# Kernel optimization log

Measured on AMD Instinct MI355X. Metric: run time of the kernel, lower is better.

## Reference

```python
import jax, jax.numpy as jnp
import numpy as np

D_MODEL = 1024
NUM_HEADS = 16
D_HEAD = D_MODEL // NUM_HEADS
BATCH = 4
SEQ = 2048
NEG_INF = -1e30


def setup_inputs() -> dict:
    key = jax.random.key(0)
    k_x, k_q, k_k, k_v, k_o = jax.random.split(key, 5)
    scale = 1.0 / np.sqrt(D_MODEL)
    x = jax.random.normal(k_x, (BATCH, SEQ, D_MODEL), dtype=jnp.float32)
    Qw = jax.random.normal(k_q, (D_MODEL, D_MODEL), dtype=jnp.float32) * scale
    Kw = jax.random.normal(k_k, (D_MODEL, D_MODEL), dtype=jnp.float32) * scale
    Vw = jax.random.normal(k_v, (D_MODEL, D_MODEL), dtype=jnp.float32) * scale
    Ow = jax.random.normal(k_o, (D_MODEL, D_MODEL), dtype=jnp.float32) * scale
    padding_mask = jnp.zeros((BATCH, SEQ), dtype=bool)  # True = masked position
    return {"x": x, "Qw": Qw, "Kw": Kw, "Vw": Vw, "Ow": Ow, "padding_mask": padding_mask}


def reference(x, Qw, Kw, Vw, Ow, padding_mask):
    B, S, D = x.shape
    H, dh = NUM_HEADS, D_HEAD
    # torch Linear (no bias): y = x @ W.T
    q = jnp.einsum("bsd,ed->bse", x, Qw).reshape(B, S, H, dh)
    k = jnp.einsum("bsd,ed->bse", x, Kw).reshape(B, S, H, dh)
    v = jnp.einsum("bsd,ed->bse", x, Vw).reshape(B, S, H, dh)
    # scores: [B, H, Sq, Sk]
    score = jnp.einsum("bqhd,bkhd->bhqk", q, k) / jnp.sqrt(jnp.float32(dh))
    # causal mask (masked=True)
    causal = jnp.tril(jnp.ones((S, S), dtype=bool))  # True = keep
    score = jnp.where(causal[None, None, :, :], score, NEG_INF)
    # padding mask: True = masked key position
    score = jnp.where(padding_mask[:, None, None, :], NEG_INF, score)
    attn = jax.nn.softmax(score, axis=-1)  # dropout=0.0 (eval mode)
    ctx = jnp.einsum("bhqk,bkhd->bqhd", attn, v).reshape(B, S, D)
    out = jnp.einsum("bsd,ed->bse", ctx, Ow)
    return out
```

## Files before the change

kernel.cpp:

```cpp
#include <hip/hip_runtime.h>
#include <hip/hip_bf16.h>

typedef __attribute__((ext_vector_type(8))) short short8;
typedef __attribute__((ext_vector_type(4))) float f32x4;

#define MFMA_BF16_16x16x32(a,b,c) __builtin_amdgcn_mfma_f32_16x16x32_bf16((a),(b),(c),0,0,0)

constexpr int B_  = 4;
constexpr int S_  = 2048;
constexpr int H_  = 16;
constexpr int DH_ = 64;
constexpr int D_  = 1024;
constexpr int M_  = B_ * S_;

__device__ __forceinline__ unsigned short f2bf(float f) {
  union { float f; unsigned u; } v; v.f = f;
  unsigned u = v.u;
  u += 0x7fffu + ((u >> 16) & 1u);
  return (unsigned short)(u >> 16);
}

__device__ __forceinline__ short8 cvt8(f32x4 a, f32x4 b) {
  union { __hip_bfloat162 h[4]; short8 s; } u;
  u.h[0] = __float22bfloat162_rn(make_float2(a[0], a[1]));
  u.h[1] = __float22bfloat162_rn(make_float2(a[2], a[3]));
  u.h[2] = __float22bfloat162_rn(make_float2(b[0], b[1]));
  u.h[3] = __float22bfloat162_rn(make_float2(b[2], b[3]));
  return u.s;
}

__global__ __launch_bounds__(256)
void gemm_qkv(const float* __restrict__ x,
              const float* __restrict__ Qw, const float* __restrict__ Kw,
              const float* __restrict__ Vw,
              unsigned short* __restrict__ Qo, unsigned short* __restrict__ Ko,
              unsigned short* __restrict__ VTo) {
  constexpr int BM = 128, BK = 32, LDK = 40;
  __shared__ __align__(16) short As[BM * LDK];
  __shared__ __align__(16) short Bs[BM * LDK];

  const int nb = blockIdx.x;
  const float* W;
  unsigned short* out;
  float scale = 1.0f;
  int epi;
  if (nb < 8)       { W = Qw; out = Qo;  scale = 0.125f; epi = 1; }
  else if (nb < 16) { W = Kw; out = Ko;  epi = 1; }
  else              { W = Vw; out = VTo; epi = 2; }

  const int tid  = threadIdx.x;
  const int lane = tid & 63;
  const int w    = tid >> 6;
  const int quad = lane >> 4;
  const int l16  = lane & 15;
  const int wm   = (w >> 1) * 64;
  const int wn   = (w & 1) * 64;

  const int m0 = blockIdx.y * BM;
  const int n0 = (nb & 7) * 128;

  f32x4 acc[4][4];
  #pragma unroll
  for (int i = 0; i < 4; ++i)
    #pragma unroll
    for (int j = 0; j < 4; ++j)
      acc[i][j] = (f32x4){0.f, 0.f, 0.f, 0.f};

  for (int k0 = 0; k0 < D_; k0 += BK) {
    __syncthreads();
    #pragma unroll
    for (int i = 0; i < 2; ++i) {
      int flat = i * 256 + tid;
      int row  = flat >> 2;
      int col  = (flat & 3) * 8;
      const float* Ap = x + (size_t)(m0 + row) * D_ + k0 + col;
      *(short8*)(&As[row * LDK + col]) = cvt8(*(const f32x4*)Ap, *(const f32x4*)(Ap + 4));
      const float* Wp = W + (size_t)(n0 + row) * D_ + k0 + col;
      *(short8*)(&Bs[row * LDK + col]) = cvt8(*(const f32x4*)Wp, *(const f32x4*)(Wp + 4));
    }
    __syncthreads();

    short8 af[4], bf[4];
    #pragma unroll
    for (int i = 0; i < 4; ++i)
      af[i] = *(const short8*)(&As[(wm + i * 16 + l16) * LDK + quad * 8]);
    #pragma unroll
    for (int j = 0; j < 4; ++j)
      bf[j] = *(const short8*)(&Bs[(wn + j * 16 + l16) * LDK + quad * 8]);
    #pragma unroll
    for (int i = 0; i < 4; ++i)
      #pragma unroll
      for (int j = 0; j < 4; ++j)
        acc[i][j] = MFMA_BF16_16x16x32(af[i], bf[j], acc[i][j]);
  }

  #pragma unroll
  for (int i = 0; i < 4; ++i)
    #pragma unroll
    for (int j = 0; j < 4; ++j)
      #pragma unroll
      for (int r = 0; r < 4; ++r) {
        int m = m0 + wm + i * 16 + quad * 4 + r;
        int n = n0 + wn + j * 16 + l16;
        unsigned short bv = f2bf(acc[i][j][r] * scale);
        int b = m >> 11, s = m & (S_ - 1);
        int h = n >> 6,  d = n & (DH_ - 1);
        if (epi == 1)
          out[((size_t)(b * H_ + h) * S_ + s) * DH_ + d] = bv;
        else
          out[((size_t)(b * H_ + h) * DH_ + d) * S_ + s] = bv;
      }
}

__global__ __launch_bounds__(256)
void gemm_out(const unsigned short* __restrict__ A,
              const float* __restrict__ W,
              float* __restrict__ out) {
  constexpr int BM = 128, BK = 32, LDK = 40;
  __shared__ __align__(16) short As[BM * LDK];
  __shared__ __align__(16) short Bs[BM * LDK];

  const int tid  = threadIdx.x;
  const int lane = tid & 63;
  const int w    = tid >> 6;
  const int quad = lane >> 4;
  const int l16  = lane & 15;
  const int wm   = (w >> 1) * 64;
  const int wn   = (w & 1) * 64;

  const int m0 = blockIdx.y * BM;
  const int n0 = blockIdx.x * 128;

  f32x4 acc[4][4];
  #pragma unroll
  for (int i = 0; i < 4; ++i)
    #pragma unroll
    for (int j = 0; j < 4; ++j)
      acc[i][j] = (f32x4){0.f, 0.f, 0.f, 0.f};

  for (int k0 = 0; k0 < D_; k0 += BK) {
    __syncthreads();
    #pragma unroll
    for (int i = 0; i < 2; ++i) {
      int flat = i * 256 + tid;
      int row  = flat >> 2;
      int col  = (flat & 3) * 8;
      *(short8*)(&As[row * LDK + col]) =
          *(const short8*)(A + (size_t)(m0 + row) * D_ + k0 + col);
      const float* Wp = W + (size_t)(n0 + row) * D_ + k0 + col;
      *(short8*)(&Bs[row * LDK + col]) = cvt8(*(const f32x4*)Wp, *(const f32x4*)(Wp + 4));
    }
    __syncthreads();

    short8 af[4], bf[4];
    #pragma unroll
    for (int i = 0; i < 4; ++i)
      af[i] = *(const short8*)(&As[(wm + i * 16 + l16) * LDK + quad * 8]);
    #pragma unroll
    for (int j = 0; j < 4; ++j)
      bf[j] = *(const short8*)(&Bs[(wn + j * 16 + l16) * LDK + quad * 8]);
    #pragma unroll
    for (int i = 0; i < 4; ++i)
      #pragma unroll
      for (int j = 0; j < 4; ++j)
        acc[i][j] = MFMA_BF16_16x16x32(af[i], bf[j], acc[i][j]);
  }

  #pragma unroll
  for (int i = 0; i < 4; ++i)
    #pragma unroll
    for (int j = 0; j < 4; ++j)
      #pragma unroll
      for (int r = 0; r < 4; ++r) {
        int m = m0 + wm + i * 16 + quad * 4 + r;
        int n = n0 + wn + j * 16 + l16;
        out[(size_t)m * D_ + n] = acc[i][j][r];
      }
}

constexpr int LDP_ = 72;

__device__ __forceinline__ void attn_range(
    const unsigned short* __restrict__ Kh,
    const unsigned short* __restrict__ Vh,
    const unsigned char* __restrict__ pmb,
    short* __restrict__ Pw,
    const short8 qf[2][2], f32x4 acc[2][4], f32x4 lacc[2],
    int qw, int kt0, int kt1, int quad, int l16) {
  const short8 ones = {0x3F80, 0x3F80, 0x3F80, 0x3F80,
                       0x3F80, 0x3F80, 0x3F80, 0x3F80};
  for (int kt = kt0; kt < kt1; ++kt) {
    const int k0 = kt * 64;

    short8 kb[8];
    #pragma unroll
    for (int t = 0; t < 4; ++t) {
      const unsigned short* kp = Kh + (size_t)(k0 + t * 16 + l16) * DH_ + quad * 8;
      kb[t * 2]     = *(const short8*)(kp);
      kb[t * 2 + 1] = *(const short8*)(kp + 32);
    }
    unsigned char pd[4];
    #pragma unroll
    for (int t = 0; t < 4; ++t) pd[t] = pmb[k0 + t * 16 + l16];

    f32x4 sc[2][4];
    __builtin_amdgcn_s_setprio(1);
    #pragma unroll
    for (int t = 0; t < 4; ++t) {
      #pragma unroll
      for (int i = 0; i < 2; ++i) {
        f32x4 z = (f32x4){0.f, 0.f, 0.f, 0.f};
        z = MFMA_BF16_16x16x32(qf[i][0], kb[t * 2], z);
        sc[i][t] = MFMA_BF16_16x16x32(qf[i][1], kb[t * 2 + 1], z);
      }
    }
    __builtin_amdgcn_s_setprio(0);

    #pragma unroll
    for (int t = 0; t < 4; ++t) {
      float pb = pd[t] ? -1e30f : 0.f;
      #pragma unroll
      for (int i = 0; i < 2; ++i)
        #pragma unroll
        for (int r = 0; r < 4; ++r)
          sc[i][t][r] += pb;
    }
    if (k0 + 63 > qw) {
      #pragma unroll
      for (int t = 0; t < 4; ++t) {
        int key = k0 + t * 16 + l16;
        #pragma unroll
        for (int i = 0; i < 2; ++i)
          #pragma unroll
          for (int r = 0; r < 4; ++r) {
            int qrow = qw + i * 16 + quad * 4 + r;
            if (key > qrow) sc[i][t][r] = -1e30f;
          }
      }
    }
    #pragma unroll
    for (int i = 0; i < 2; ++i)
      #pragma unroll
      for (int t = 0; t < 4; ++t)
        #pragma unroll
        for (int r = 0; r < 4; ++r)
          sc[i][t][r] = __expf(sc[i][t][r]);

    #pragma unroll
    for (int i = 0; i < 2; ++i)
      #pragma unroll
      for (int t = 0; t < 4; ++t)
        #pragma unroll
        for (int r = 0; r < 4; ++r)
          Pw[(i * 16 + quad * 4 + r) * LDP_ + t * 16 + l16] = (short)f2bf(sc[i][t][r]);

    short8 vb[8];
    #pragma unroll
    for (int ks = 0; ks < 2; ++ks)
      #pragma unroll
      for (int t = 0; t < 4; ++t)
        vb[ks * 4 + t] = *(const short8*)(Vh + (size_t)(t * 16 + l16) * S_ +
                                          k0 + ks * 32 + quad * 8);

    __builtin_amdgcn_s_setprio(1);
    #pragma unroll
    for (int ks = 0; ks < 2; ++ks) {
      short8 pa0 = *(const short8*)(&Pw[l16 * LDP_ + ks * 32 + quad * 8]);
      short8 pa1 = *(const short8*)(&Pw[(16 + l16) * LDP_ + ks * 32 + quad * 8]);
      #pragma unroll
      for (int t = 0; t < 4; ++t) {
        acc[0][t] = MFMA_BF16_16x16x32(pa0, vb[ks * 4 + t], acc[0][t]);
        acc[1][t] = MFMA_BF16_16x16x32(pa1, vb[ks * 4 + t], acc[1][t]);
      }
      lacc[0] = MFMA_BF16_16x16x32(pa0, ones, lacc[0]);
      lacc[1] = MFMA_BF16_16x16x32(pa1, ones, lacc[1]);
    }
    __builtin_amdgcn_s_setprio(0);
  }
}

__global__ __launch_bounds__(128)
void attn(const unsigned short* __restrict__ Q,
          const unsigned short* __restrict__ K,
          const unsigned short* __restrict__ VT,
          const unsigned char* __restrict__ pmask,
          unsigned short* __restrict__ CTX) {
  __shared__ __align__(16) short Ps[2 * 32 * LDP_];
  __shared__ float Rbuf[64 * 40];

  const int tid  = threadIdx.x;
  const int lane = tid & 63;
  const int w    = tid >> 6;
  const int quad = lane >> 4;
  const int l16  = lane & 15;

  const int L    = blockIdx.x;
  const int xcd  = L & 7;
  const int slot = L >> 3;
  const int bh   = xcd + 8 * (slot & 7);
  const int p    = slot >> 3;
  const int b    = bh >> 4;
  const int h    = bh & 15;

  const int qtA = p, qtB = 63 - p;
  const int ntA = (qtA >> 1) + 1;
  const int ntB = (qtB >> 1) + 1;
  const int splitB = 17 - ntA;

  const unsigned short* Qh = Q  + ((size_t)b * H_ + h) * S_ * DH_;
  const unsigned short* Kh = K  + ((size_t)b * H_ + h) * S_ * DH_;
  const unsigned short* Vh = VT + ((size_t)b * H_ + h) * DH_ * S_;
  const unsigned char* pmb = pmask + (size_t)b * S_;
  unsigned short* CTXb = CTX + (size_t)b * S_ * D_;
  short* Pw = &Ps[w * 32 * LDP_];

  f32x4 acc[2][4];
  f32x4 lacc[2];
  short8 qf[2][2];

  if (w == 0) {
    {
      const int qw = qtA * 32;
      #pragma unroll
      for (int i = 0; i < 2; ++i)
        #pragma unroll
        for (int c = 0; c < 2; ++c)
          qf[i][c] = *(const short8*)(Qh + (size_t)(qw + i * 16 + l16) * DH_ + c * 32 + quad * 8);
      #pragma unroll
      for (int i = 0; i < 2; ++i) {
        #pragma unroll
        for (int t = 0; t < 4; ++t) acc[i][t] = (f32x4){0.f, 0.f, 0.f, 0.f};
        lacc[i] = (f32x4){0.f, 0.f, 0.f, 0.f};
      }
      attn_range(Kh, Vh, pmb, Pw, qf, acc, lacc, qw, 0, ntA, quad, l16);
      #pragma unroll
      for (int i = 0; i < 2; ++i)
        #pragma unroll
        for (int r = 0; r < 4; ++r) {
          int qrow = qw + i * 16 + quad * 4 + r;
          float inv = 1.0f / lacc[i][r];
          #pragma unroll
          for (int t = 0; t < 4; ++t)
            CTXb[(size_t)qrow * D_ + h * DH_ + t * 16 + l16] = f2bf(acc[i][t][r] * inv);
        }
    }
    {
      const int qw = qtB * 32;
      #pragma unroll
      for (int i = 0; i < 2; ++i)
        #pragma unroll
        for (int c = 0; c < 2; ++c)
          qf[i][c] = *(const short8*)(Qh + (size_t)(qw + i * 16 + l16) * DH_ + c * 32 + quad * 8);
      #pragma unroll
      for (int i = 0; i < 2; ++i) {
        #pragma unroll
        for (int t = 0; t < 4; ++t) acc[i][t] = (f32x4){0.f, 0.f, 0.f, 0.f};
        lacc[i] = (f32x4){0.f, 0.f, 0.f, 0.f};
      }
      attn_range(Kh, Vh, pmb, Pw, qf, acc, lacc, qw, 0, splitB, quad, l16);
      __syncthreads();
      #pragma unroll
      for (int i = 0; i < 2; ++i) {
        #pragma unroll
        for (int t = 0; t < 4; ++t)
          #pragma unroll
          for (int r = 0; r < 4; ++r)
            acc[i][t][r] += Rbuf[lane * 40 + i * 16 + t * 4 + r];
        #pragma unroll
        for (int r = 0; r < 4; ++r)
          lacc[i][r] += Rbuf[lane * 40 + 32 + i * 4 + r];
      }
      #pragma unroll
      for (int i = 0; i < 2; ++i)
        #pragma unroll
        for (int r = 0; r < 4; ++r) {
          int qrow = qw + i * 16 + quad * 4 + r;
          float inv = 1.0f / lacc[i][r];
          #pragma unroll
          for (int t = 0; t < 4; ++t)
            CTXb[(size_t)qrow * D_ + h * DH_ + t * 16 + l16] = f2bf(acc[i][t][r] * inv);
        }
    }
  } else {
    const int qw = qtB * 32;
    #pragma unroll
    for (int i = 0; i < 2; ++i)
      #pragma unroll
      for (int c = 0; c < 2; ++c)
        qf[i][c] = *(const short8*)(Qh + (size_t)(qw + i * 16 + l16) * DH_ + c * 32 + quad * 8);
    #pragma unroll
    for (int i = 0; i < 2; ++i) {
      #pragma unroll
      for (int t = 0; t < 4; ++t) acc[i][t] = (f32x4){0.f, 0.f, 0.f, 0.f};
      lacc[i] = (f32x4){0.f, 0.f, 0.f, 0.f};
    }
    attn_range(Kh, Vh, pmb, Pw, qf, acc, lacc, qw, splitB, ntB, quad, l16);
    #pragma unroll
    for (int i = 0; i < 2; ++i) {
      #pragma unroll
      for (int t = 0; t < 4; ++t)
        #pragma unroll
        for (int r = 0; r < 4; ++r)
          Rbuf[lane * 40 + i * 16 + t * 4 + r] = acc[i][t][r];
      #pragma unroll
      for (int r = 0; r < 4; ++r)
        Rbuf[lane * 40 + 32 + i * 4 + r] = lacc[i][r];
    }
    __syncthreads();
  }
}

extern "C" void kernel_launch(void* const* d_in, const int* in_sizes, int n_in,
                              void* d_out, int out_size, void* d_ws, size_t ws_size,
                              hipStream_t stream) {
  const float* x  = (const float*)d_in[0];
  const float* Qw = (const float*)d_in[1];
  const float* Kw = (const float*)d_in[2];
  const float* Vw = (const float*)d_in[3];
  const float* Ow = (const float*)d_in[4];
  const unsigned char* pm = (const unsigned char*)d_in[5];

  const size_t NE = (size_t)M_ * D_;
  unsigned short* Qall  = (unsigned short*)d_out;
  unsigned short* CTXa  = (unsigned short*)d_out + NE;
  unsigned short* Kall  = (unsigned short*)d_ws;
  unsigned short* VTall = (unsigned short*)d_ws + NE;

  gemm_qkv<<<dim3(24, M_ / 128), 256, 0, stream>>>(x, Qw, Kw, Vw,
                                                   Qall, Kall, VTall);

  attn<<<dim3(2048), 128, 0, stream>>>(Qall, Kall, VTall, pm, CTXa);

  hipMemcpyAsync(d_ws, (const void*)CTXa, NE * sizeof(unsigned short),
                 hipMemcpyDeviceToDevice, stream);

  gemm_out<<<dim3(D_ / 128, M_ / 128), 256, 0, stream>>>((unsigned short*)d_ws,
                                                         Ow, (float*)d_out);
}
```

Baseline: 374.1 us.

## Pre-convert x to bf16 and transpose score MFMA for packed P stores

```diff
diff --git a/kernel.cpp b/kernel.cpp
--- a/kernel.cpp
+++ b/kernel.cpp
@@ -29,8 +29,22 @@
   return u.s;
 }
 
+__device__ __forceinline__ unsigned pk2(float a, float b) {
+  union { __hip_bfloat162 h; unsigned u; } z;
+  z.h = __float22bfloat162_rn(make_float2(a, b));
+  return z.u;
+}
+
 __global__ __launch_bounds__(256)
-void gemm_qkv(const float* __restrict__ x,
+void cvt_x(const float* __restrict__ x, unsigned short* __restrict__ xb) {
+  const size_t i = ((size_t)blockIdx.x * 256 + threadIdx.x) * 8;
+  f32x4 a = *(const f32x4*)(x + i);
+  f32x4 b = *(const f32x4*)(x + i + 4);
+  *(short8*)(xb + i) = cvt8(a, b);
+}
+
+__global__ __launch_bounds__(256)
+void gemm_qkv(const unsigned short* __restrict__ xb,
               const float* __restrict__ Qw, const float* __restrict__ Kw,
               const float* __restrict__ Vw,
               unsigned short* __restrict__ Qo, unsigned short* __restrict__ Ko,
@@ -73,8 +87,8 @@
       int flat = i * 256 + tid;
       int row  = flat >> 2;
       int col  = (flat & 3) * 8;
-      const float* Ap = x + (size_t)(m0 + row) * D_ + k0 + col;
-      *(short8*)(&As[row * LDK + col]) = cvt8(*(const f32x4*)Ap, *(const f32x4*)(Ap + 4));
+      *(short8*)(&As[row * LDK + col]) =
+          *(const short8*)(xb + (size_t)(m0 + row) * D_ + k0 + col);
       const float* Wp = W + (size_t)(n0 + row) * D_ + k0 + col;
       *(short8*)(&Bs[row * LDK + col]) = cvt8(*(const f32x4*)Wp, *(const f32x4*)(Wp + 4));
     }
@@ -199,9 +213,10 @@
       kb[t * 2]     = *(const short8*)(kp);
       kb[t * 2 + 1] = *(const short8*)(kp + 32);
     }
-    unsigned char pd[4];
-    #pragma unroll
-    for (int t = 0; t < 4; ++t) pd[t] = pmb[k0 + t * 16 + l16];
+    unsigned pm4[4];
+    #pragma unroll
+    for (int t = 0; t < 4; ++t)
+      pm4[t] = *(const unsigned*)(pmb + k0 + t * 16 + quad * 4);
 
     f32x4 sc[2][4];
     __builtin_amdgcn_s_setprio(1);
@@ -210,57 +225,52 @@
       #pragma unroll
       for (int i = 0; i < 2; ++i) {
         f32x4 z = (f32x4){0.f, 0.f, 0.f, 0.f};
-        z = MFMA_BF16_16x16x32(qf[i][0], kb[t * 2], z);
-        sc[i][t] = MFMA_BF16_16x16x32(qf[i][1], kb[t * 2 + 1], z);
+        z = MFMA_BF16_16x16x32(kb[t * 2], qf[i][0], z);
+        sc[i][t] = MFMA_BF16_16x16x32(kb[t * 2 + 1], qf[i][1], z);
       }
     }
     __builtin_amdgcn_s_setprio(0);
 
-    #pragma unroll
-    for (int t = 0; t < 4; ++t) {
-      float pb = pd[t] ? -1e30f : 0.f;
-      #pragma unroll
-      for (int i = 0; i < 2; ++i)
-        #pragma unroll
-        for (int r = 0; r < 4; ++r)
-          sc[i][t][r] += pb;
-    }
+    short8 vb[8];
+    #pragma unroll
+    for (int t = 0; t < 4; ++t)
+      vb[t] = *(const short8*)(Vh + (size_t)(t * 16 + l16) * S_ + k0 + quad * 8);
+
+    #pragma unroll
+    for (int i = 0; i < 2; ++i)
+      #pragma unroll
+      for (int t = 0; t < 4; ++t)
+        #pragma unroll
+        for (int r = 0; r < 4; ++r) {
+          float e = __expf(sc[i][t][r]);
+          sc[i][t][r] = ((pm4[t] >> (8 * r)) & 0xffu) ? 0.f : e;
+        }
     if (k0 + 63 > qw) {
       #pragma unroll
+      for (int t = 0; t < 4; ++t)
+        #pragma unroll
+        for (int r = 0; r < 4; ++r) {
+          int key = k0 + t * 16 + quad * 4 + r;
+          #pragma unroll
+          for (int i = 0; i < 2; ++i) {
+            int qrow = qw + i * 16 + l16;
+            if (key > qrow) sc[i][t][r] = 0.f;
+          }
+        }
+    }
+
+    #pragma unroll
+    for (int i = 0; i < 2; ++i)
+      #pragma unroll
       for (int t = 0; t < 4; ++t) {
-        int key = k0 + t * 16 + l16;
-        #pragma unroll
-        for (int i = 0; i < 2; ++i)
-          #pragma unroll
-          for (int r = 0; r < 4; ++r) {
-            int qrow = qw + i * 16 + quad * 4 + r;
-            if (key > qrow) sc[i][t][r] = -1e30f;
-          }
-      }
-    }
-    #pragma unroll
-    for (int i = 0; i < 2; ++i)
-      #pragma unroll
-      for (int t = 0; t < 4; ++t)
-        #pragma unroll
-        for (int r = 0; r < 4; ++r)
-          sc[i][t][r] = __expf(sc[i][t][r]);
-
-    #pragma unroll
-    for (int i = 0; i < 2; ++i)
-      #pragma unroll
-      for (int t = 0; t < 4; ++t)
-        #pragma unroll
-        for (int r = 0; r < 4; ++r)
-          Pw[(i * 16 + quad * 4 + r) * LDP_ + t * 16 + l16] = (short)f2bf(sc[i][t][r]);
-
-    short8 vb[8];
-    #pragma unroll
-    for (int ks = 0; ks < 2; ++ks)
-      #pragma unroll
-      for (int t = 0; t < 4; ++t)
-        vb[ks * 4 + t] = *(const short8*)(Vh + (size_t)(t * 16 + l16) * S_ +
-                                          k0 + ks * 32 + quad * 8);
+        unsigned lo = pk2(sc[i][t][0], sc[i][t][1]);
+        unsigned hi = pk2(sc[i][t][2], sc[i][t][3]);
+        *(uint2*)(&Pw[(i * 16 + l16) * LDP_ + t * 16 + quad * 4]) = make_uint2(lo, hi);
+      }
+
+    #pragma unroll
+    for (int t = 0; t < 4; ++t)
+      vb[4 + t] = *(const short8*)(Vh + (size_t)(t * 16 + l16) * S_ + k0 + 32 + quad * 8);
 
     __builtin_amdgcn_s_setprio(1);
     #pragma unroll
@@ -426,7 +436,9 @@
   unsigned short* Kall  = (unsigned short*)d_ws;
   unsigned short* VTall = (unsigned short*)d_ws + NE;
 
-  gemm_qkv<<<dim3(24, M_ / 128), 256, 0, stream>>>(x, Qw, Kw, Vw,
+  cvt_x<<<dim3((M_ * D_) / (256 * 8)), 256, 0, stream>>>(x, CTXa);
+
+  gemm_qkv<<<dim3(24, M_ / 128), 256, 0, stream>>>(CTXa, Qw, Kw, Vw,
                                                    Qall, Kall, VTall);
 
   attn<<<dim3(2048), 128, 0, stream>>>(Qall, Kall, VTall, pm, CTXa);
```

Measured after the change: 373.7 us. Within noise of the previous version (-0.1%).
